# Kernel optimization log

Measured on AMD Instinct MI355X. Metric: run time of the kernel, lower is better.

Reference implementation:

```python
import jax, jax.numpy as jnp
import numpy as np

KS = 3                 # kernel_size
DILATIONS = (1, 2, 3)  # dilation list
NUM_HEADS = 6


def _unfold_reflect(x, ks, dil):
    """ReflectionPad2d(dil*(ks-1)//2) + Unfold(ks, dilation=dil).
    x: [B, C, H, W] -> [B, C*ks*ks, H, W] (channel-major like torch Unfold)."""
    pad = dil * (ks - 1) // 2
    xp = jnp.pad(x, ((0, 0), (0, 0), (pad, pad), (pad, pad)), mode='reflect')
    return jax.lax.conv_general_dilated_patches(
        xp, filter_shape=(ks, ks), window_strides=(1, 1), padding='VALID',
        rhs_dilation=(dil, dil))  # [B, C*ks*ks, H, W]


def _dilate_attention(q, k, v, head_dim, ks, dil):
    """q,k,v: [B, c2, H, W] -> [B, H, W, c2]."""
    B, c2, H, W = q.shape
    nh = c2 // head_dim
    scale = head_dim ** (-0.5)
    P = H * W
    k2 = ks * ks
    # q -> [B, nh, P, hd]
    qr = q.reshape(B, nh, head_dim, P).transpose(0, 1, 3, 2)
    # unfold k, v -> [B, c2*k2, H, W], channel order (c, kh, kw)
    ku = _unfold_reflect(k, ks, dil).reshape(B, nh, head_dim, k2, P)
    vu = _unfold_reflect(v, ks, dil).reshape(B, nh, head_dim, k2, P)
    kr = ku.transpose(0, 1, 4, 2, 3)  # [B, nh, P, hd, k2]
    vr = vu.transpose(0, 1, 4, 3, 2)  # [B, nh, P, k2, hd]
    scores = jnp.einsum('bnpd,bnpdk->bnpk', qr, kr) * scale
    attn = jax.nn.softmax(scores, axis=-1)
    out = jnp.einsum('bnpk,bnpkd->bnpd', attn, vr)  # [B, nh, P, hd]
    return out.transpose(0, 2, 1, 3).reshape(B, H, W, nh * head_dim)


def _forward(x, pos_w, pos_b, qkv_w, proj_w):
    B, C, H, W = x.shape
    nd = len(DILATIONS)
    c2 = C // nd
    head_dim = C // NUM_HEADS
    # depthwise 3x3 positional conv (groups=C) + residual
    pe = jax.lax.conv_general_dilated(
        x, pos_w, window_strides=(1, 1), padding=((1, 1), (1, 1)),
        dimension_numbers=('NCHW', 'OIHW', 'NCHW'), feature_group_count=C)
    x = x + pe + pos_b[None, :, None, None]
    # 1x1 qkv conv
    qkv = jnp.einsum('oc,bchw->bohw', qkv_w, x)  # [B, 3C, H, W]
    # 'b (three nd c2) h w -> nd three b c2 h w'
    qkv = qkv.reshape(B, 3, nd, c2, H, W).transpose(2, 1, 0, 3, 4, 5)
    outs = []
    for i, dil in enumerate(DILATIONS):
        o = _dilate_attention(qkv[i, 0], qkv[i, 1], qkv[i, 2], head_dim, KS, dil)
        outs.append(o.transpose(0, 3, 1, 2))  # [B, c2, H, W]
    xo = jnp.concatenate(outs, axis=1)  # [B, C, H, W], dilation-major channels
    return jnp.einsum('oc,bchw->bohw', proj_w, xo)


def setup_inputs() -> dict:
    key = jax.random.key(0)
    ks = jax.random.split(key, 5)
    B, C, H, W = 4, 192, 128, 128
    return {
        'x': jax.random.normal(ks[0], (B, C, H, W), dtype=jnp.float32),
        'pos_w': jax.random.normal(ks[1], (C, 1, 3, 3), dtype=jnp.float32) * 0.05,
        'pos_b': jax.random.normal(ks[2], (C,), dtype=jnp.float32) * 0.05,
        'qkv_w': jax.random.normal(ks[3], (3 * C, C), dtype=jnp.float32) * (C ** -0.5),
        'proj_w': jax.random.normal(ks[4], (C, C), dtype=jnp.float32) * (C ** -0.5),
    }


def reference(x, pos_w, pos_b, qkv_w, proj_w):
    return _forward(x, pos_w, pos_b, qkv_w, proj_w)
```

## Files before the change

kernel.cpp:

```cpp
#include <hip/hip_runtime.h>
#include <hip/hip_bf16.h>
#include <math.h>

#define Hdim 128
#define Wdim 128
#define HW   16384
#define Cdim 192
#define Bdim 4
#define QKVC 576
#define NTOT (Bdim * HW)

typedef __attribute__((ext_vector_type(8))) short short8;
typedef __attribute__((ext_vector_type(4))) short short4v;
typedef __attribute__((ext_vector_type(4))) float f32x4;

__device__ __forceinline__ void async_ld16(void* lds, const void* g) {
    __builtin_amdgcn_global_load_lds(
        (const __attribute__((address_space(1))) void*)g,
        (__attribute__((address_space(3))) void*)lds, 16, 0, 0);
}
__device__ __forceinline__ float lo16(unsigned u) { return __uint_as_float(u << 16); }
__device__ __forceinline__ float hi16(unsigned u) { return __uint_as_float(u & 0xffff0000u); }

__global__ void convert_w(const float* __restrict__ qkv_w,
                          const float* __restrict__ proj_w,
                          __hip_bfloat16* __restrict__ Wq,
                          __hip_bfloat16* __restrict__ Wp) {
    int i = blockIdx.x * 256 + threadIdx.x;
    if (i < QKVC * Cdim) {
        Wq[i] = __float2bfloat16(qkv_w[i]);
    } else {
        int j = i - QKVC * Cdim;
        Wp[j] = __float2bfloat16(proj_w[j]);
    }
}

__global__ __launch_bounds__(256, 5)
void posconv_nhwc(const float* __restrict__ x,
                  const float* __restrict__ pos_w,
                  const float* __restrict__ pos_b,
                  __hip_bfloat16* __restrict__ Xb) {
    __shared__ __align__(16) float xs[3 * 16 * 128];
    __shared__ __hip_bfloat16 tile[16][132];

    int t = threadIdx.x;
    int id = blockIdx.x;
    int xj = id & 7;
    int r_ = id >> 3;
    int rb = r_ & 15;
    int cg = (r_ >> 4) % 12;
    int b  = (r_ >> 4) / 12;
    int h  = xj * 16 + rb;

    int hh0 = h > 0 ? h - 1 : 0;
    int hh1 = h;
    int hh2 = h < Hdim - 1 ? h + 1 : Hdim - 1;

    int ch = t >> 4;
    int qh = t & 15;
    int cglob = cg * 16 + ch;

    const float* wp = pos_w + cglob * 9;
    float w0 = wp[0], w1 = wp[1], w2 = wp[2];
    float w3 = wp[3], w4 = wp[4], w5 = wp[5];
    float w6 = wp[6], w7 = wp[7], w8 = wp[8];
    float bias = pos_b[cglob];
    float m0 = (h > 0) ? 1.f : 0.f;
    float m2 = (h < Hdim - 1) ? 1.f : 0.f;
    w0 *= m0; w1 *= m0; w2 *= m0;
    w6 *= m2; w7 *= m2; w8 *= m2;

    {
        const float* xg = x + (size_t)(b * Cdim + cg * 16) * HW;
#pragma unroll
        for (int k = 0; k < 6; ++k) {
            int u = t + k * 256;
            int rowi = u >> 5;
            int ql = u & 31;
            int rr = rowi >> 4;
            int sch = rowi & 15;
            int hr = rr == 0 ? hh0 : (rr == 1 ? hh1 : hh2);
            int qs = ql ^ sch;
            async_ld16((char*)xs + (size_t)u * 16,
                       xg + (size_t)sch * HW + hr * Wdim + qs * 4);
        }
    }
    __syncthreads();

    float out[8];
    {
        const char* xsb = (const char*)xs;
        const char* r0b = xsb + (size_t)(0 * 16 + ch) * 512;
        const char* r1b = xsb + (size_t)(1 * 16 + ch) * 512;
        const char* r2b = xsb + (size_t)(2 * 16 + ch) * 512;
        float4 lo0 = *(const float4*)(r0b + (((2 * qh)     ^ ch) * 16));
        float4 hi0 = *(const float4*)(r0b + (((2 * qh + 1) ^ ch) * 16));
        float4 lo1 = *(const float4*)(r1b + (((2 * qh)     ^ ch) * 16));
        float4 hi1 = *(const float4*)(r1b + (((2 * qh + 1) ^ ch) * 16));
        float4 lo2 = *(const float4*)(r2b + (((2 * qh)     ^ ch) * 16));
        float4 hi2 = *(const float4*)(r2b + (((2 * qh + 1) ^ ch) * 16));
        float L0 = __shfl_up(hi0.w, 1, 64), R0 = __shfl_down(lo0.x, 1, 64);
        float L1 = __shfl_up(hi1.w, 1, 64), R1 = __shfl_down(lo1.x, 1, 64);
        float L2 = __shfl_up(hi2.w, 1, 64), R2 = __shfl_down(lo2.x, 1, 64);
        if (qh == 0)  { L0 = 0.f; L1 = 0.f; L2 = 0.f; }
        if (qh == 15) { R0 = 0.f; R1 = 0.f; R2 = 0.f; }
        float a0[10] = {L0, lo0.x, lo0.y, lo0.z, lo0.w, hi0.x, hi0.y, hi0.z, hi0.w, R0};
        float a1[10] = {L1, lo1.x, lo1.y, lo1.z, lo1.w, hi1.x, hi1.y, hi1.z, hi1.w, R1};
        float a2[10] = {L2, lo2.x, lo2.y, lo2.z, lo2.w, hi2.x, hi2.y, hi2.z, hi2.w, R2};
#pragma unroll
        for (int i = 0; i < 8; ++i) {
            out[i] = a1[i + 1] + bias
                   + w0 * a0[i] + w1 * a0[i + 1] + w2 * a0[i + 2]
                   + w3 * a1[i] + w4 * a1[i + 1] + w5 * a1[i + 2]
                   + w6 * a2[i] + w7 * a2[i + 1] + w8 * a2[i + 2];
        }
    }

    union { unsigned short u[8]; short8 v; } pk;
#pragma unroll
    for (int i = 0; i < 8; ++i) {
        __hip_bfloat16 bv = __float2bfloat16(out[i]);
        pk.u[i] = *(unsigned short*)&bv;
    }
    *(short8*)(void*)&tile[ch][qh * 8] = pk.v;
    __syncthreads();

    int px = t >> 1, s2 = t & 1;
    union { unsigned short u[8]; short8 v; } o;
#pragma unroll
    for (int j = 0; j < 8; ++j)
        o.u[j] = *(const unsigned short*)&tile[s2 * 8 + j][px];
    size_t p0img = (size_t)(b << 14) + (size_t)h * Wdim;
    *(short8*)(void*)(Xb + (p0img + px) * Cdim + cg * 16 + s2 * 8) = o.v;
}

template <int MODE, int MT>
__global__ __launch_bounds__(256, 3)
void gemm_mfma(const __hip_bfloat16* __restrict__ Wb,
               const __hip_bfloat16* __restrict__ Xt,
               void* __restrict__ Cout) {
    __shared__ __hip_bfloat16 As[2][64 * 32];
    __shared__ __hip_bfloat16 Bs[2][256 * 32];
    const int t = threadIdx.x;
    const int w = t >> 6, l = t & 63;
    const int lq = l >> 4, lr = l & 15;
    const int id = blockIdx.x;
    const int xj = id & 7;
    const int rest = id >> 3;
    const int m0 = (rest % MT) * 64;
    const int n0 = ((rest / MT) * 8 + xj) * 256;

    const int ms = t >> 2, kcs = t & 3;

    auto stage = [&](int buf, int kt_) {
        const int k0_ = kt_ * 32;
        async_ld16(As[buf] + t * 8,
                   Wb + (size_t)(m0 + ms) * Cdim + k0_ + kcs * 8);
#pragma unroll
        for (int it = 0; it < 4; ++it) {
            int idx = it * 256 + t;
            int n = idx >> 2, kc = idx & 3;
            const __hip_bfloat16* src;
            if (MODE == 0)
                src = Xt + (size_t)(n0 + n) * Cdim + k0_ + kc * 8;
            else
                src = Xt + (size_t)kt_ * ((size_t)NTOT * 32) +
                      (size_t)(n0 + n) * 32 + kc * 8;
            async_ld16(Bs[buf] + idx * 8, src);
        }
    };

    f32x4 acc[4][4] = {};

    stage(0, 0);
    __syncthreads();

#pragma unroll
    for (int kt = 0; kt < 6; ++kt) {
        const int cur = kt & 1;
        if (kt < 5) stage(cur ^ 1, kt + 1);

        short8 af[4], bf[4];
#pragma unroll
        for (int i = 0; i < 4; ++i)
            af[i] = *(const short8*)(void*)(As[cur] + (i * 16 + lr) * 32 + lq * 8);
#pragma unroll
        for (int j = 0; j < 4; ++j)
            bf[j] = *(const short8*)(void*)(Bs[cur] + (w * 64 + j * 16 + lr) * 32 + lq * 8);
#pragma unroll
        for (int i = 0; i < 4; ++i)
#pragma unroll
            for (int j = 0; j < 4; ++j)
                acc[i][j] = __builtin_amdgcn_mfma_f32_16x16x32_bf16(
                    af[i], bf[j], acc[i][j], 0, 0, 0);

        __syncthreads();
    }

#pragma unroll
    for (int i = 0; i < 4; ++i) {
        int mb = m0 + i * 16 + lq * 4;
#pragma unroll
        for (int j = 0; j < 4; ++j) {
            int n = n0 + w * 64 + j * 16 + lr;
            if (MODE == 0) {
                int three = mb / 192, rem = mb % 192;
                int pi = rem >> 6, pn = (rem >> 5) & 1, d4 = rem & 31;
                size_t plane = (size_t)((three * 3 + pi) * 2 + pn);
                __hip_bfloat16* dst = (__hip_bfloat16*)Cout +
                    plane * ((size_t)NTOT * 32) + (size_t)n * 32 + d4;
                short4v pk;
#pragma unroll
                for (int r = 0; r < 4; ++r) {
                    __hip_bfloat16 bv = __float2bfloat16(acc[i][j][r]);
                    pk[r] = *(short*)&bv;
                }
                *(short4v*)(void*)dst = pk;
            } else {
                int b = n >> 14, p = n & (HW - 1);
#pragma unroll
                for (int r = 0; r < 4; ++r)
                    ((float*)Cout)[((size_t)(b * Cdim + mb + r)) * HW + p] =
                        acc[i][j][r];
            }
        }
    }
}

__global__ __launch_bounds__(512, 2)
void attn_proj(const __hip_bfloat16* __restrict__ QKV,
               const __hip_bfloat16* __restrict__ Wpg,
               float* __restrict__ out) {
    __shared__ __align__(16) unsigned char smem[76800];
    unsigned char* kv  = smem;
    unsigned char* wpl = smem;

    const int t = threadIdx.x;
    const int px = t >> 2, s = t & 3;
    const int id = blockIdx.x;
    const int xj = id & 7, rest = id >> 3;
    const int b = rest >> 4, rb = rest & 15;
    const int h = xj * 16 + rb;
    const size_t PS = (size_t)NTOT * 32;
    const size_t colbase = (size_t)(b << 14) + (size_t)h * Wdim;

    uint4 qv[6];
#pragma unroll
    for (int c = 0; c < 6; ++c)
        qv[c] = *((const uint4*)(QKV + (size_t)c * PS + (colbase + px) * 32) + s);

    const int g = t ^ ((t >> 3) & 7);

    auto stageKV = [&](int comb) {
        int dil = (comb >> 1) + 1;
#pragma unroll
        for (int kh = 0; kh < 3; ++kh) {
            int v = h + (kh - 1) * dil;
            v = v < 0 ? -v : (v >= Hdim ? 2 * Hdim - 2 - v : v);
            size_t rowe = ((size_t)(b << 14) + (size_t)v * Wdim) * 32;
            async_ld16(kv + (kh * 512 + t) * 16,
                       QKV + (size_t)(6 + comb) * PS + rowe + g * 8);
            async_ld16(kv + ((kh + 3) * 512 + t) * 16,
                       QKV + (size_t)(12 + comb) * PS + rowe + g * 8);
        }
    };

    unsigned pa[6][4];

    stageKV(0);
    __syncthreads();

#pragma unroll
    for (int c = 0; c < 6; ++c) {
        {
            const int dil = (c >> 1) + 1;
            float q[8];
            {
                uint4 x = qv[c];
                q[0] = lo16(x.x); q[1] = hi16(x.x);
                q[2] = lo16(x.y); q[3] = hi16(x.y);
                q[4] = lo16(x.z); q[5] = hi16(x.z);
                q[6] = lo16(x.w); q[7] = hi16(x.w);
            }
            int coff[3];
#pragma unroll
            for (int kw = 0; kw < 3; ++kw) {
                int ww = px + (kw - 1) * dil;
                ww = ww < 0 ? -ww : (ww >= Wdim ? 2 * Wdim - 2 - ww : ww);
                int i0 = 4 * ww + s;
                coff[kw] = (i0 ^ ((i0 >> 3) & 7)) * 16;
            }
            float sc[9];
#pragma unroll
            for (int kh = 0; kh < 3; ++kh)
#pragma unroll
                for (int kw = 0; kw < 3; ++kw) {
                    uint4 xk = *(const uint4*)(void*)(kv + kh * 8192 + coff[kw]);
                    sc[kh * 3 + kw] =
                          q[0] * lo16(xk.x) + q[1] * hi16(xk.x)
                        + q[2] * lo16(xk.y) + q[3] * hi16(xk.y)
                        + q[4] * lo16(xk.z) + q[5] * hi16(xk.z)
                        + q[6] * lo16(xk.w) + q[7] * hi16(xk.w);
                }
#pragma unroll
            for (int j = 0; j < 9; ++j) {
                float v = sc[j];
                v += __shfl_xor(v, 1, 64);
                v += __shfl_xor(v, 2, 64);
                sc[j] = v * 0.17677669529663687f;
            }
            float mx = sc[0];
#pragma unroll
            for (int j = 1; j < 9; ++j) mx = fmaxf(mx, sc[j]);
            float sum = 0.f;
#pragma unroll
            for (int j = 0; j < 9; ++j) { sc[j] = __expf(sc[j] - mx); sum += sc[j]; }
            float inv = 1.f / sum;

            float a8[8] = {};
#pragma unroll
            for (int kh = 0; kh < 3; ++kh)
#pragma unroll
                for (int kw = 0; kw < 3; ++kw) {
                    float a = sc[kh * 3 + kw];
                    uint4 xv = *(const uint4*)(void*)(kv + (kh + 3) * 8192 + coff[kw]);
                    a8[0] += a * lo16(xv.x); a8[1] += a * hi16(xv.x);
                    a8[2] += a * lo16(xv.y); a8[3] += a * hi16(xv.y);
                    a8[4] += a * lo16(xv.z); a8[5] += a * hi16(xv.z);
                    a8[6] += a * lo16(xv.w); a8[7] += a * hi16(xv.w);
                }
#pragma unroll
            for (int j = 0; j < 4; ++j) {
                __hip_bfloat16 blo = __float2bfloat16(a8[2 * j]     * inv);
                __hip_bfloat16 bhi = __float2bfloat16(a8[2 * j + 1] * inv);
                pa[c][j] = (unsigned)*(unsigned short*)&blo |
                           ((unsigned)*(unsigned short*)&bhi << 16);
            }
        }
        __syncthreads();
        if (c < 5) {
            stageKV(c + 1);
            __syncthreads();
        }
    }

#pragma unroll
    for (int k = 0; k < 10; ++k) {
        if (k < 9 || t < 192) {
            int cidx = t + k * 512;
            int row = cidx / 25, cc = cidx - row * 25;
            async_ld16(wpl + (size_t)cidx * 16, Wpg + row * 192 + cc * 8);
        }
    }
    __syncthreads();

    const int wv = t >> 6, l = t & 63;
    const int lq = l >> 4, lr = l & 15;
    const int srcl = (l & 15) * 4 + (l >> 4);
    f32x4 pacc[12] = {};
#pragma unroll
    for (int kt = 0; kt < 6; ++kt) {
        union { unsigned d[4]; short8 v; } bu;
#pragma unroll
        for (int j = 0; j < 4; ++j)
            bu.d[j] = (unsigned)__shfl((int)pa[kt][j], srcl, 64);
        short8 bfrag = bu.v;
#pragma unroll
        for (int i = 0; i < 12; ++i) {
            short8 afrag = *(const short8*)(void*)
                (wpl + (size_t)((i * 16 + lr) * 25 + kt * 4 + lq) * 16);
            pacc[i] = __builtin_amdgcn_mfma_f32_16x16x32_bf16(
                afrag, bfrag, pacc[i], 0, 0, 0);
        }
    }
    float* outp = out + (size_t)b * Cdim * HW + (size_t)h * Wdim;
#pragma unroll
    for (int i = 0; i < 12; ++i) {
        int o = i * 16 + lq * 4;
        int pxn = wv * 16 + lr;
#pragma unroll
        for (int r = 0; r < 4; ++r)
            outp[(size_t)(o + r) * HW + pxn] = pacc[i][r];
    }
}

extern "C" void kernel_launch(void* const* d_in, const int* in_sizes, int n_in,
                              void* d_out, int out_size, void* d_ws, size_t ws_size,
                              hipStream_t stream) {
    const float* x      = (const float*)d_in[0];
    const float* pos_w  = (const float*)d_in[1];
    const float* pos_b  = (const float*)d_in[2];
    const float* qkv_w  = (const float*)d_in[3];
    const float* proj_w = (const float*)d_in[4];
    float* out = (float*)d_out;

    char* ws = (char*)d_ws;
    __hip_bfloat16* Xb  = (__hip_bfloat16*)ws;
    __hip_bfloat16* QKV = (__hip_bfloat16*)(ws + (size_t)25165824);
    __hip_bfloat16* Wq  = (__hip_bfloat16*)(ws + (size_t)125829120);
    __hip_bfloat16* Wp  = (__hip_bfloat16*)(ws + (size_t)126050304);

    convert_w<<<(QKVC * Cdim + Cdim * Cdim) / 256, 256, 0, stream>>>(
        qkv_w, proj_w, Wq, Wp);

    posconv_nhwc<<<6144, 256, 0, stream>>>(x, pos_w, pos_b, Xb);

    gemm_mfma<0, 9><<<2304, 256, 0, stream>>>(Wq, Xb, QKV);

    attn_proj<<<512, 512, 0, stream>>>(QKV, Wp, out);
}
```

Before: 208.5 us.

## Split attention blocks into half-row tiles and stream projection weights in thirds

The fused attention+projection kernel now processes half an image row per block: 256 threads, 1024 blocks, with a K/V halo of 72 columns staged in LDS. Attention outputs go to an LDS buffer instead of staying in registers and being shuffled. The projection weights are loaded and applied in three 64-row chunks, which lowers LDS use (53KB vs 77KB) and register pressure so more blocks fit per CU. In exchange there are extra halo loads, more barriers, and repeated weight staging.

```diff
diff --git a/kernel.cpp b/kernel.cpp
--- a/kernel.cpp
+++ b/kernel.cpp
@@ -227,45 +227,57 @@
     }
 }
 
-__global__ __launch_bounds__(512, 2)
+__global__ __launch_bounds__(256, 3)
 void attn_proj(const __hip_bfloat16* __restrict__ QKV,
                const __hip_bfloat16* __restrict__ Wpg,
                float* __restrict__ out) {
-    __shared__ __align__(16) unsigned char smem[76800];
+    __shared__ __align__(16) unsigned char smem[53248];
     unsigned char* kv  = smem;
+    unsigned char* aob = smem + 27648;
     unsigned char* wpl = smem;
 
     const int t = threadIdx.x;
-    const int px = t >> 2, s = t & 3;
+    const int pxl = t >> 2, s = t & 3;
     const int id = blockIdx.x;
     const int xj = id & 7, rest = id >> 3;
-    const int b = rest >> 4, rb = rest & 15;
-    const int h = xj * 16 + rb;
+    const int b = rest >> 5;
+    const int k5 = rest & 31;
+    const int h = xj * 16 + (k5 >> 1);
+    const int w0 = (k5 & 1) * 64;
+    const int ws = (w0 == 0) ? 0 : 56;
     const size_t PS = (size_t)NTOT * 32;
     const size_t colbase = (size_t)(b << 14) + (size_t)h * Wdim;
 
     uint4 qv[6];
 #pragma unroll
     for (int c = 0; c < 6; ++c)
-        qv[c] = *((const uint4*)(QKV + (size_t)c * PS + (colbase + px) * 32) + s);
-
-    const int g = t ^ ((t >> 3) & 7);
+        qv[c] = *((const uint4*)(QKV + (size_t)c * PS +
+                                 (colbase + w0 + pxl) * 32) + s);
 
     auto stageKV = [&](int comb) {
         int dil = (comb >> 1) + 1;
+        int hh[3];
 #pragma unroll
         for (int kh = 0; kh < 3; ++kh) {
             int v = h + (kh - 1) * dil;
-            v = v < 0 ? -v : (v >= Hdim ? 2 * Hdim - 2 - v : v);
-            size_t rowe = ((size_t)(b << 14) + (size_t)v * Wdim) * 32;
-            async_ld16(kv + (kh * 512 + t) * 16,
-                       QKV + (size_t)(6 + comb) * PS + rowe + g * 8);
-            async_ld16(kv + ((kh + 3) * 512 + t) * 16,
-                       QKV + (size_t)(12 + comb) * PS + rowe + g * 8);
+            hh[kh] = v < 0 ? -v : (v >= Hdim ? 2 * Hdim - 2 - v : v);
+        }
+#pragma unroll
+        for (int k = 0; k < 7; ++k) {
+            if (k < 6 || t < 192) {
+                int c = t + k * 256;
+                int r = c / 288;
+                int cc = c - r * 288;
+                int kh = (r >= 3) ? r - 3 : r;
+                int plane = (r >= 3) ? 12 + comb : 6 + comb;
+                int gc = cc ^ ((cc >> 3) & 7);
+                size_t rowe = ((size_t)(b << 14) +
+                               (size_t)hh[kh] * Wdim + ws) * 32;
+                async_ld16(kv + (size_t)c * 16,
+                           QKV + (size_t)plane * PS + rowe + gc * 8);
+            }
         }
     };
-
-    unsigned pa[6][4];
 
     stageKV(0);
     __syncthreads();
@@ -285,9 +297,9 @@
             int coff[3];
 #pragma unroll
             for (int kw = 0; kw < 3; ++kw) {
-                int ww = px + (kw - 1) * dil;
+                int ww = w0 + pxl + (kw - 1) * dil;
                 ww = ww < 0 ? -ww : (ww >= Wdim ? 2 * Wdim - 2 - ww : ww);
-                int i0 = 4 * ww + s;
+                int i0 = 4 * (ww - ws) + s;
                 coff[kw] = (i0 ^ ((i0 >> 3) & 7)) * 16;
             }
             float sc[9];
@@ -295,7 +307,7 @@
             for (int kh = 0; kh < 3; ++kh)
 #pragma unroll
                 for (int kw = 0; kw < 3; ++kw) {
-                    uint4 xk = *(const uint4*)(void*)(kv + kh * 8192 + coff[kw]);
+                    uint4 xk = *(const uint4*)(void*)(kv + kh * 4608 + coff[kw]);
                     sc[kh * 3 + kw] =
                           q[0] * lo16(xk.x) + q[1] * hi16(xk.x)
                         + q[2] * lo16(xk.y) + q[3] * hi16(xk.y)
@@ -323,19 +335,20 @@
 #pragma unroll
                 for (int kw = 0; kw < 3; ++kw) {
                     float a = sc[kh * 3 + kw];
-                    uint4 xv = *(const uint4*)(void*)(kv + (kh + 3) * 8192 + coff[kw]);
+                    uint4 xv = *(const uint4*)(void*)
+                        (kv + (kh + 3) * 4608 + coff[kw]);
                     a8[0] += a * lo16(xv.x); a8[1] += a * hi16(xv.x);
                     a8[2] += a * lo16(xv.y); a8[3] += a * hi16(xv.y);
                     a8[4] += a * lo16(xv.z); a8[5] += a * hi16(xv.z);
                     a8[6] += a * lo16(xv.w); a8[7] += a * hi16(xv.w);
                 }
-#pragma unroll
-            for (int j = 0; j < 4; ++j) {
-                __hip_bfloat16 blo = __float2bfloat16(a8[2 * j]     * inv);
-                __hip_bfloat16 bhi = __float2bfloat16(a8[2 * j + 1] * inv);
-                pa[c][j] = (unsigned)*(unsigned short*)&blo |
-                           ((unsigned)*(unsigned short*)&bhi << 16);
-            }
+            union { unsigned short u[8]; short8 v; } pk;
+#pragma unroll
+            for (int d2 = 0; d2 < 8; ++d2) {
+                __hip_bfloat16 bv = __float2bfloat16(a8[d2] * inv);
+                pk.u[d2] = *(unsigned short*)&bv;
+            }
+            *(short8*)(void*)(aob + pxl * 400 + c * 64 + s * 16) = pk.v;
         }
         __syncthreads();
         if (c < 5) {
@@ -344,43 +357,48 @@
         }
     }
 
-#pragma unroll
-    for (int k = 0; k < 10; ++k) {
-        if (k < 9 || t < 192) {
-            int cidx = t + k * 512;
-            int row = cidx / 25, cc = cidx - row * 25;
-            async_ld16(wpl + (size_t)cidx * 16, Wpg + row * 192 + cc * 8);
-        }
-    }
-    __syncthreads();
-
     const int wv = t >> 6, l = t & 63;
     const int lq = l >> 4, lr = l & 15;
-    const int srcl = (l & 15) * 4 + (l >> 4);
-    f32x4 pacc[12] = {};
-#pragma unroll
-    for (int kt = 0; kt < 6; ++kt) {
-        union { unsigned d[4]; short8 v; } bu;
-#pragma unroll
-        for (int j = 0; j < 4; ++j)
-            bu.d[j] = (unsigned)__shfl((int)pa[kt][j], srcl, 64);
-        short8 bfrag = bu.v;
-#pragma unroll
-        for (int i = 0; i < 12; ++i) {
-            short8 afrag = *(const short8*)(void*)
-                (wpl + (size_t)((i * 16 + lr) * 25 + kt * 4 + lq) * 16);
-            pacc[i] = __builtin_amdgcn_mfma_f32_16x16x32_bf16(
-                afrag, bfrag, pacc[i], 0, 0, 0);
-        }
-    }
-    float* outp = out + (size_t)b * Cdim * HW + (size_t)h * Wdim;
-#pragma unroll
-    for (int i = 0; i < 12; ++i) {
-        int o = i * 16 + lq * 4;
-        int pxn = wv * 16 + lr;
-#pragma unroll
-        for (int r = 0; r < 4; ++r)
-            outp[(size_t)(o + r) * HW + pxn] = pacc[i][r];
+    const int pxn = wv * 16 + lr;
+    float* outp = out + (size_t)b * Cdim * HW + (size_t)h * Wdim + w0;
+
+    short8 bfr[6];
+#pragma unroll
+    for (int kt = 0; kt < 6; ++kt)
+        bfr[kt] = *(const short8*)(void*)(aob + pxn * 400 + kt * 64 + lq * 16);
+
+#pragma unroll
+    for (int third = 0; third < 3; ++third) {
+#pragma unroll
+        for (int k = 0; k < 7; ++k) {
+            if (k < 6 || t < 64) {
+                int c = t + k * 256;
+                int row = c / 25, cc = c - row * 25;
+                async_ld16(wpl + (size_t)c * 16,
+                           Wpg + (third * 64 + row) * 192 + cc * 8);
+            }
+        }
+        __syncthreads();
+
+        f32x4 pacc[4] = {};
+#pragma unroll
+        for (int kt = 0; kt < 6; ++kt) {
+#pragma unroll
+            for (int i2 = 0; i2 < 4; ++i2) {
+                short8 afrag = *(const short8*)(void*)
+                    (wpl + (size_t)((i2 * 16 + lr) * 25 + kt * 4 + lq) * 16);
+                pacc[i2] = __builtin_amdgcn_mfma_f32_16x16x32_bf16(
+                    afrag, bfr[kt], pacc[i2], 0, 0, 0);
+            }
+        }
+#pragma unroll
+        for (int i2 = 0; i2 < 4; ++i2) {
+            int o = third * 64 + i2 * 16 + lq * 4;
+#pragma unroll
+            for (int r = 0; r < 4; ++r)
+                outp[(size_t)(o + r) * HW + pxn] = pacc[i2][r];
+        }
+        if (third < 2) __syncthreads();
     }
 }
 
@@ -407,5 +425,5 @@
 
     gemm_mfma<0, 9><<<2304, 256, 0, stream>>>(Wq, Xb, QKV);
 
-    attn_proj<<<512, 512, 0, stream>>>(QKV, Wp, out);
-}
+    attn_proj<<<1024, 256, 0, stream>>>(QKV, Wp, out);
+}
```

Result: faster. 172.8 us (-17.1%).
